# Optimization experiments

Measured on AMD Instinct MI355X. Metric: run time of the kernel, lower is better.

## Reference

```python
import jax, jax.numpy as jnp
import numpy as np

H = 1024
B, LK, LQ = 16, 2048, 64


def setup_inputs() -> dict:
    key0 = jax.random.key(0)
    ks = jax.random.split(key0, 16)
    f = jax.random.normal
    return {
        "query": f(ks[0], (B, 1, H), jnp.float32),
        "key": f(ks[1], (B, LK, 2 * H), jnp.float32),
        "value": f(ks[2], (B, LK, 2 * H), jnp.float32),
        "mask": jax.random.randint(ks[3], (B, 1, LK), 0, 2).astype(jnp.int32),
        "q_key": f(ks[4], (B, LQ, 2 * H), jnp.float32),
        "q_value": f(ks[5], (B, LQ, 2 * H), jnp.float32),
        "q_mask": jax.random.randint(ks[6], (B, 1, LQ), 0, 2).astype(jnp.int32),
        "alphas_state": jax.random.uniform(ks[7], (B, 1, LK), jnp.float32),
        "q_alphas_state": jax.random.uniform(ks[8], (B, 1, LQ), jnp.float32),
        # nn.Linear params: W is [out, in], y = x @ W.T + b
        "W_q": f(ks[9], (2 * H, H + 2 * H + 1), jnp.float32) * 0.02,
        "b_q": jnp.zeros((2 * H,), jnp.float32),
        "W_t": f(ks[10], (2 * H, H + 2 * H + 1 + 2 * H), jnp.float32) * 0.02,
        "b_t": jnp.zeros((2 * H,), jnp.float32),
        "query_other": jax.random.uniform(ks[11], (1, 2 * H), jnp.float32, minval=-0.005, maxval=0.005),
        "text_other": jax.random.uniform(ks[12], (1, 2 * H), jnp.float32, minval=-0.005, maxval=0.005),
    }


def reference(query, key, value, mask, q_key, q_value, q_mask,
              alphas_state, q_alphas_state,
              W_q, b_q, W_t, b_t, query_other, text_other):
    neg_inf = jnp.float32(-jnp.inf)
    Bq, Lq, _ = q_key.shape
    Bk, Lk, _ = key.shape
    # ---- query-side additive attention ----
    qrep = jnp.broadcast_to(query, (Bq, Lq, query.shape[-1]))            # repeat(1, Lq, 1)
    feat = jnp.concatenate([q_key, qrep, q_alphas_state.reshape(Bq, Lq, 1)], axis=-1)
    h = jnp.tanh(jnp.einsum('bli,oi->blo', feat, W_q) + b_q)             # [B, Lq, 2H]
    scores = jnp.einsum('blo,o->bl', h, query_other[0])[:, None, :]      # fused per-batch loop -> [B,1,Lq]
    scores = jnp.where(q_mask == 0, neg_inf, scores)
    q_alphas = jax.nn.softmax(scores, axis=-1)
    query_loss = jnp.sum(jnp.min(
        jnp.concatenate([q_alphas_state[:, 0, :], q_alphas[:, 0, :]], axis=0), axis=0))
    q_context = jnp.einsum('bql,bld->bqd', q_alphas, q_value)            # bmm -> [B,1,2H]
    # ---- text-side additive attention ----
    qrep_k = jnp.broadcast_to(query, (Bk, Lk, query.shape[-1]))
    ctx_rep = jnp.broadcast_to(q_context, (Bk, Lk, q_context.shape[-1]))
    feat_t = jnp.concatenate([key, qrep_k, alphas_state.reshape(Bk, Lk, 1), ctx_rep], axis=-1)
    h_t = jnp.tanh(jnp.einsum('bli,oi->blo', feat_t, W_t) + b_t)         # [B, Lk, 2H]
    scores_t = jnp.einsum('blo,o->bl', h_t, text_other[0])[:, None, :]   # [B,1,Lk]
    scores_t = jnp.where(mask == 0, neg_inf, scores_t)
    alphas = jax.nn.softmax(scores_t, axis=-1)
    text_loss = jnp.sum(jnp.min(
        jnp.concatenate([alphas_state[:, 0, :], alphas[:, 0, :]], axis=0), axis=0))
    context = jnp.einsum('bql,bld->bqd', alphas, value)                  # [B,1,2H]
    return (context, alphas, q_alphas, text_loss, query_loss)
```

## Files before the change

kernel.cpp:

```cpp
#include <hip/hip_runtime.h>
#include <hip/hip_bf16.h>
#include <math.h>

#define GK 2048
#define NCB 16

typedef __attribute__((ext_vector_type(8))) short bf16x8;
typedef __attribute__((ext_vector_type(4))) float f32x4;
typedef __attribute__((ext_vector_type(4))) float f4v;
typedef __attribute__((ext_vector_type(4))) unsigned short u16x4;
typedef __attribute__((ext_vector_type(8))) unsigned short u16x8;

__device__ __forceinline__ unsigned short f2bf(float x) {
    unsigned int u = __float_as_uint(x);
    u += 0x7fffu + ((u >> 16) & 1u);
    return (unsigned short)(u >> 16);
}

__device__ __forceinline__ void gl_lds16(const void* g, void* l) {
    __builtin_amdgcn_global_load_lds(
        (const __attribute__((address_space(1))) unsigned int*)g,
        (__attribute__((address_space(3))) unsigned int*)l, 16, 0, 0);
}

__global__ void prep_kernel(const float* __restrict__ Wt, const float* __restrict__ Wq,
                            const float* __restrict__ q_key, const float* __restrict__ key,
                            const float* __restrict__ query, const float* __restrict__ b_q,
                            unsigned short* __restrict__ Wtk, unsigned short* __restrict__ Wqk,
                            unsigned short* __restrict__ qkb, unsigned short* __restrict__ keyb,
                            float* __restrict__ w3q, float* __restrict__ w3t,
                            float* __restrict__ Dq) {
    int b = blockIdx.x, tid = threadIdx.x;
    if (b < 32768) {
        long i = ((long)b << 11) + (tid << 3);
        f4v a = *(const f4v*)(key + i);
        f4v c = *(const f4v*)(key + i + 4);
        u16x8 r;
        r[0] = f2bf(a[0]); r[1] = f2bf(a[1]); r[2] = f2bf(a[2]); r[3] = f2bf(a[3]);
        r[4] = f2bf(c[0]); r[5] = f2bf(c[1]); r[6] = f2bf(c[2]); r[7] = f2bf(c[3]);
        *(u16x8*)(keyb + i) = r;
        return;
    }
    int b2 = b - 32768;
    if (b2 < 2048) {
        const float* s = Wt + (size_t)b2 * 5121;
        unsigned short* d = Wtk + (size_t)b2 * 2048;
#pragma unroll
        for (int k = 0; k < 8; k++) { int c = tid + (k << 8); d[c] = f2bf(s[c]); }
    } else if (b2 < 4096) {
        int o = b2 - 2048;
        const float* s = Wq + (size_t)o * 3073;
        unsigned short* d = Wqk + (size_t)o * 2048;
#pragma unroll
        for (int k = 0; k < 8; k++) { int c = tid + (k << 8); d[c] = f2bf(s[c]); }
    } else if (b2 < 5120) {
        long i = ((long)(b2 - 4096) * 256 + tid) * 8;
        f4v a = *(const f4v*)(q_key + i);
        f4v c = *(const f4v*)(q_key + i + 4);
        u16x8 r;
        r[0] = f2bf(a[0]); r[1] = f2bf(a[1]); r[2] = f2bf(a[2]); r[3] = f2bf(a[3]);
        r[4] = f2bf(c[0]); r[5] = f2bf(c[1]); r[6] = f2bf(c[2]); r[7] = f2bf(c[3]);
        *(u16x8*)(qkb + i) = r;
    } else if (b2 < 5128) {
        int o = (b2 - 5120) * 256 + tid;
        w3q[o] = Wq[(size_t)o * 3073 + 3072];
        w3t[o] = Wt[(size_t)o * 5121 + 3072];
    } else {
        int wave = tid >> 6, lane = tid & 63;
        int o = (b2 - 5128) * 4 + wave;
        const float* wrow = Wq + (size_t)o * 3073 + 2048;
        float acc[16];
#pragma unroll
        for (int z = 0; z < 16; z++) acc[z] = 0.f;
        for (int i = lane; i < 1024; i += 64) {
            float wv = wrow[i];
            const float* qp = query + i;
#pragma unroll
            for (int z = 0; z < 16; z++) acc[z] += wv * qp[z * 1024];
        }
#pragma unroll
        for (int z = 0; z < 16; z++) {
            float v = acc[z];
            for (int off = 1; off < 64; off <<= 1) v += __shfl_xor(v, off);
            if (lane == 0) Dq[(z << 11) + o] = v + b_q[o];
        }
    }
}

template <int KLEN>
__global__ __launch_bounds__(256) void dconst_kernel(
    const float* __restrict__ W, long ldw,
    const float* __restrict__ bias,
    const float* __restrict__ query,
    const float* __restrict__ qctx,
    float* __restrict__ Dout) {
    int tid = threadIdx.x;
    int wave = tid >> 6, lane = tid & 63;
    int o = blockIdx.x * 4 + wave;
    const float* wrow = W + (size_t)o * ldw + 2048;
    float acc[16];
#pragma unroll
    for (int b2 = 0; b2 < 16; b2++) acc[b2] = 0.f;
    for (int i = lane; i < KLEN; i += 64) {
        if (KLEN == 1024 || i < 1024) {
            float wv = wrow[i];
            const float* qp = query + i;
#pragma unroll
            for (int b2 = 0; b2 < 16; b2++) acc[b2] += wv * qp[b2 * 1024];
        } else {
            float wv = wrow[i + 1];
            const float* cp = qctx + (i - 1024);
#pragma unroll
            for (int b2 = 0; b2 < 16; b2++) acc[b2] += wv * cp[b2 * 2048];
        }
    }
#pragma unroll
    for (int b2 = 0; b2 < 16; b2++) {
        float v = acc[b2];
        for (int off = 1; off < 64; off <<= 1) v += __shfl_xor(v, off);
        if (lane == 0) Dout[(b2 << 11) + o] = v + bias[o];
    }
}

template <int LOG_RPB>
__global__ __launch_bounds__(256) void gemm_score(
    const unsigned short* __restrict__ A,
    const unsigned short* __restrict__ Bt,
    const float* __restrict__ Dc,
    const float* __restrict__ avec,
    const float* __restrict__ w3,
    const float* __restrict__ tvec,
    float* __restrict__ partial,
    int row0) {
    __shared__ unsigned short As[128 * 32];
    __shared__ unsigned short Bs[128 * 32];
    __shared__ float red[128][2];

    int nwg = gridDim.x;
    int bid = blockIdx.x;
    int q8 = nwg >> 3;
    int wg = (bid & 7) * q8 + (bid >> 3);
    int rb = wg >> 4, cb = wg & 15;

    int tid = threadIdx.x;
    int wave = tid >> 6, lane = tid & 63;
    int wr = wave >> 1, wc = wave & 1;
    int l15 = lane & 15, lhi = lane >> 4;

    const unsigned short* Ab = A + (size_t)rb * 128 * GK;
    const unsigned short* Bb = Bt + (size_t)cb * 128 * GK;

    int r0 = tid >> 2, c0 = (tid & 3) << 3;

    f32x4 acc[4][4];
#pragma unroll
    for (int i = 0; i < 4; i++)
#pragma unroll
        for (int j = 0; j < 4; j++) acc[i][j] = (f32x4)0.f;

    unsigned short* AsW0 = As + (wave << 9);
    unsigned short* AsW1 = As + 2048 + (wave << 9);
    unsigned short* BsW0 = Bs + (wave << 9);
    unsigned short* BsW1 = Bs + 2048 + (wave << 9);

    for (int k0 = 0; k0 < GK; k0 += 32) {
        __syncthreads();
        gl_lds16(Ab + (size_t)r0 * GK + k0 + c0, AsW0);
        gl_lds16(Ab + (size_t)(r0 + 64) * GK + k0 + c0, AsW1);
        gl_lds16(Bb + (size_t)r0 * GK + k0 + c0, BsW0);
        gl_lds16(Bb + (size_t)(r0 + 64) * GK + k0 + c0, BsW1);
        __syncthreads();
        bf16x8 a[4], b[4];
#pragma unroll
        for (int mi = 0; mi < 4; mi++)
            a[mi] = *(const bf16x8*)(As + (((wr << 6) + (mi << 4) + l15) << 5) + (lhi << 3));
#pragma unroll
        for (int ni = 0; ni < 4; ni++)
            b[ni] = *(const bf16x8*)(Bs + (((wc << 6) + (ni << 4) + l15) << 5) + (lhi << 3));
#pragma unroll
        for (int mi = 0; mi < 4; mi++)
#pragma unroll
            for (int ni = 0; ni < 4; ni++)
                acc[mi][ni] = __builtin_amdgcn_mfma_f32_16x16x32_bf16(a[mi], b[ni], acc[mi][ni], 0, 0, 0);
    }

    int grow_base = row0 + (rb << 7) + (wr << 6);
    int bb = grow_base >> LOG_RPB;
    int gcol = (cb << 7) + (wc << 6) + l15;
    float Dco[4], w3o[4], tv[4];
#pragma unroll
    for (int ni = 0; ni < 4; ni++) {
        int o = gcol + (ni << 4);
        Dco[ni] = Dc[(bb << 11) + o];
        w3o[ni] = w3[o];
        tv[ni] = tvec[o];
    }
#pragma unroll
    for (int mi = 0; mi < 4; mi++) {
#pragma unroll
        for (int j = 0; j < 4; j++) {
            int rloc = (mi << 4) + (lhi << 2) + j;
            float av = avec[grow_base + rloc];
            float s = 0.f;
#pragma unroll
            for (int ni = 0; ni < 4; ni++) {
                float x = acc[mi][ni][j] + Dco[ni] + av * w3o[ni];
                x = fminf(fmaxf(x, -15.f), 15.f);
                float e = __expf(2.f * x);
                s += ((e - 1.f) / (e + 1.f)) * tv[ni];
            }
#pragma unroll
            for (int off = 1; off < 16; off <<= 1) s += __shfl_xor(s, off);
            if (l15 == 0) red[(wr << 6) + rloc][wc] = s;
        }
    }
    __syncthreads();
    if (tid < 128) {
        partial[(size_t)(row0 + (rb << 7) + tid) * NCB + cb] = red[tid][0] + red[tid][1];
    }
}

#define MFMA16(A, B, C) __builtin_amdgcn_mfma_f32_16x16x32_bf16(A, B, C, 0, 0, 0)

#define STAGE2(GB, GR0, K0, LB) do { \
    int _rr = lane >> 3; \
    int _cc = ((lane & 7) ^ _rr) << 3; \
    gl_lds16((GB) + (size_t)((GR0) + (wid << 3) + _rr) * GK + (K0) + _cc, lds + (LB) + (wid << 9)); \
    gl_lds16((GB) + (size_t)((GR0) + 64 + (wid << 3) + _rr) * GK + (K0) + _cc, lds + (LB) + 4096 + (wid << 9)); \
  } while (0)

#define WAIT4 do { asm volatile("s_waitcnt vmcnt(4)" ::: "memory"); __builtin_amdgcn_sched_barrier(0); } while (0)
#define NOWAIT do { } while (0)

#define PHASE(YOFF, Q, FIRSTB, STAGE_STMT, BOUNDARY) do { \
    bf16x8 a00, a01, a10, a11; \
    if (FIRSTB) { \
        b00 = *(const bf16x8*)(lds8 + bB0[0] + (YOFF)); b01 = *(const bf16x8*)(lds8 + bB1[0] + (YOFF)); \
        b10 = *(const bf16x8*)(lds8 + bB0[1] + (YOFF)); b11 = *(const bf16x8*)(lds8 + bB1[1] + (YOFF)); \
        b20 = *(const bf16x8*)(lds8 + bB0[2] + (YOFF)); b21 = *(const bf16x8*)(lds8 + bB1[2] + (YOFF)); \
        b30 = *(const bf16x8*)(lds8 + bB0[3] + (YOFF)); b31 = *(const bf16x8*)(lds8 + bB1[3] + (YOFF)); \
    } \
    a00 = *(const bf16x8*)(lds8 + aA0[2*(Q)  ] + (YOFF)); a01 = *(const bf16x8*)(lds8 + aA1[2*(Q)  ] + (YOFF)); \
    a10 = *(const bf16x8*)(lds8 + aA0[2*(Q)+1] + (YOFF)); a11 = *(const bf16x8*)(lds8 + aA1[2*(Q)+1] + (YOFF)); \
    STAGE_STMT; \
    BOUNDARY; \
    __builtin_amdgcn_s_barrier(); \
    asm volatile("s_waitcnt lgkmcnt(0)" ::: "memory"); \
    __builtin_amdgcn_sched_barrier(0); \
    __builtin_amdgcn_s_setprio(1); \
    acc[2*(Q)  ][0] = MFMA16(a00, b00, acc[2*(Q)  ][0]); \
    acc[2*(Q)  ][0] = MFMA16(a01, b01, acc[2*(Q)  ][0]); \
    acc[2*(Q)  ][1] = MFMA16(a00, b10, acc[2*(Q)  ][1]); \
    acc[2*(Q)  ][1] = MFMA16(a01, b11, acc[2*(Q)  ][1]); \
    acc[2*(Q)  ][2] = MFMA16(a00, b20, acc[2*(Q)  ][2]); \
    acc[2*(Q)  ][2] = MFMA16(a01, b21, acc[2*(Q)  ][2]); \
    acc[2*(Q)  ][3] = MFMA16(a00, b30, acc[2*(Q)  ][3]); \
    acc[2*(Q)  ][3] = MFMA16(a01, b31, acc[2*(Q)  ][3]); \
    acc[2*(Q)+1][0] = MFMA16(a10, b00, acc[2*(Q)+1][0]); \
    acc[2*(Q)+1][0] = MFMA16(a11, b01, acc[2*(Q)+1][0]); \
    acc[2*(Q)+1][1] = MFMA16(a10, b10, acc[2*(Q)+1][1]); \
    acc[2*(Q)+1][1] = MFMA16(a11, b11, acc[2*(Q)+1][1]); \
    acc[2*(Q)+1][2] = MFMA16(a10, b20, acc[2*(Q)+1][2]); \
    acc[2*(Q)+1][2] = MFMA16(a11, b21, acc[2*(Q)+1][2]); \
    acc[2*(Q)+1][3] = MFMA16(a10, b30, acc[2*(Q)+1][3]); \
    acc[2*(Q)+1][3] = MFMA16(a11, b31, acc[2*(Q)+1][3]); \
    __builtin_amdgcn_s_setprio(0); \
  } while (0)

__global__ __launch_bounds__(512, 2) void gemm256(
    const unsigned short* __restrict__ A,
    const unsigned short* __restrict__ Bt,
    const float* __restrict__ Dc,
    const float* __restrict__ avec,
    const float* __restrict__ w3,
    const float* __restrict__ tvec,
    float* __restrict__ partial) {
    extern __shared__ unsigned short lds[];
    char* lds8 = (char*)lds;
    const int XA = 0, YA = 16384, XB = 32768, YB = 49152;

    int nwg = gridDim.x;
    int bid = blockIdx.x;
    int q8 = nwg >> 3;
    int wg = (bid & 7) * q8 + (bid >> 3);
    int rb = wg >> 3, cb = wg & 7;

    int tid = threadIdx.x;
    int wid = tid >> 6, lane = tid & 63;
    int wr = wid >> 2, wc = wid & 3;
    int l15 = lane & 15, lhi = lane >> 4;

    const unsigned short* Aq = A;
    const unsigned short* Bq = Bt;
    int arow = rb << 8;
    int brow = cb << 8;

    int sw0 = ((lhi ^ (l15 & 7)) << 4);
    int sw1 = (((4 | lhi) ^ (l15 & 7)) << 4);
    int aA0[8], aA1[8], bB0[4], bB1[4];
#pragma unroll
    for (int mi = 0; mi < 8; mi++) {
        int r = (wr << 7) + (mi << 4) + l15;
        aA0[mi] = (r << 7) + sw0;
        aA1[mi] = (r << 7) + sw1;
    }
#pragma unroll
    for (int ni = 0; ni < 4; ni++) {
        int r = (wc << 6) + (ni << 4) + l15;
        bB0[ni] = 65536 + (r << 7) + sw0;
        bB1[ni] = 65536 + (r << 7) + sw1;
    }

    f32x4 acc[8][4];
#pragma unroll
    for (int i = 0; i < 8; i++)
#pragma unroll
        for (int j = 0; j < 4; j++) acc[i][j] = (f32x4)0.f;

    bf16x8 b00, b01, b10, b11, b20, b21, b30, b31;

    STAGE2(Bq, brow, 0, XB);
    STAGE2(Bq, brow + 128, 0, XB + 8192);
    STAGE2(Aq, arow, 0, XA);
    STAGE2(Aq, arow + 128, 0, XA + 8192);
    STAGE2(Bq, brow, 64, YB);
    STAGE2(Bq, brow + 128, 64, YB + 8192);
    asm volatile("s_waitcnt vmcnt(4)" ::: "memory");
    __builtin_amdgcn_sched_barrier(0);
    __builtin_amdgcn_s_barrier();

    for (int it = 0; it < 16; ++it) {
        int k1 = ((it << 1) + 1) << 6;
        int k2 = (((it << 1) + 2) << 6) & 2047;
        int k3 = (((it << 1) + 3) << 6) & 2047;
        PHASE(0,     0, 1, STAGE2(Aq, arow,       k1, YA),        NOWAIT);
        PHASE(0,     1, 0, STAGE2(Aq, arow + 128, k1, YA + 8192), NOWAIT);
        PHASE(0,     2, 0, STAGE2(Bq, brow,       k2, XB),        NOWAIT);
        PHASE(0,     3, 0, STAGE2(Bq, brow + 128, k2, XB + 8192), WAIT4);
        PHASE(32768, 0, 1, STAGE2(Aq, arow,       k2, XA),        NOWAIT);
        PHASE(32768, 1, 0, STAGE2(Aq, arow + 128, k2, XA + 8192), NOWAIT);
        PHASE(32768, 2, 0, STAGE2(Bq, brow,       k3, YB),        NOWAIT);
        PHASE(32768, 3, 0, STAGE2(Bq, brow + 128, k3, YB + 8192), WAIT4);
    }

    int gcolb = (cb << 8) + (wc << 6) + l15;
    int bb = rb >> 3;
    float Dco[4], w3o[4], tv[4];
#pragma unroll
    for (int ni = 0; ni < 4; ++ni) {
        int o = gcolb + (ni << 4);
        Dco[ni] = Dc[(bb << 11) + o];
        w3o[ni] = w3[o];
        tv[ni] = tvec[o];
    }
    float* red = (float*)(lds + 65536);
#pragma unroll
    for (int mi = 0; mi < 8; ++mi) {
#pragma unroll
        for (int j = 0; j < 4; ++j) {
            int rloc = (wr << 7) + (mi << 4) + (lhi << 2) + j;
            float av = avec[(rb << 8) + rloc];
            float s = 0.f;
#pragma unroll
            for (int ni = 0; ni < 4; ++ni) {
                float x = acc[mi][ni][j] + Dco[ni] + av * w3o[ni];
                x = fminf(fmaxf(x, -15.f), 15.f);
                float e = __expf(2.f * x);
                s += ((e - 1.f) / (e + 1.f)) * tv[ni];
            }
#pragma unroll
            for (int off2 = 1; off2 < 16; off2 <<= 1) s += __shfl_xor(s, off2);
            if (l15 == 0) red[(rloc << 2) + wc] = s;
        }
    }
    __syncthreads();
    if (tid < 256) {
        partial[(size_t)((rb << 8) + tid) * 8 + cb] =
            red[(tid << 2)] + red[(tid << 2) + 1] + red[(tid << 2) + 2] + red[(tid << 2) + 3];
    }
}

__global__ void softmax_q_alphas(const float* __restrict__ partial_q,
                                 const int* __restrict__ q_mask,
                                 float* __restrict__ out_qalphas) {
    int b = blockIdx.x, tid = threadIdx.x;
    float s = 0.f;
    const float* p = partial_q + (size_t)(b * 64 + tid) * NCB;
#pragma unroll
    for (int c = 0; c < 16; c++) s += p[c];
    if (q_mask[b * 64 + tid] == 0) s = -INFINITY;
    float m = s;
    for (int off = 1; off < 64; off <<= 1) m = fmaxf(m, __shfl_xor(m, off));
    float e = (s == -INFINITY) ? 0.f : __expf(s - m);
    float sum = e;
    for (int off = 1; off < 64; off <<= 1) sum += __shfl_xor(sum, off);
    out_qalphas[b * 64 + tid] = e / sum;
}

__global__ __launch_bounds__(256) void qctx_kernel(
    const float* __restrict__ qal, const float* __restrict__ q_value,
    float* __restrict__ qctx) {
    int b = blockIdx.x, dc = blockIdx.y, tid = threadIdx.x;
    __shared__ float sal[64];
    if (tid < 64) sal[tid] = qal[b * 64 + tid];
    __syncthreads();
    int d = (dc << 8) + tid;
    float acc = 0.f;
    for (int l = 0; l < 64; l++) {
        float al = sal[l];
        if (al != 0.f) acc += al * q_value[((size_t)(b * 64 + l) << 11) + d];
    }
    qctx[(b << 11) + d] = acc;
}

__global__ __launch_bounds__(256) void softmax_t_kernel(
    const float* __restrict__ partial,
    const int* __restrict__ mask,
    float* __restrict__ out_alphas) {
    int b = blockIdx.x, tid = threadIdx.x;
    int wave = tid >> 6, lane = tid & 63;
    __shared__ float sred[4];
    float sc[8];
    float lm = -INFINITY;
#pragma unroll
    for (int i = 0; i < 8; i++) {
        int l = tid + (i << 8);
        const float* p = partial + (size_t)(b * 2048 + l) * 8;
        float s = 0.f;
#pragma unroll
        for (int c = 0; c < 8; c++) s += p[c];
        if (mask[b * 2048 + l] == 0) s = -INFINITY;
        sc[i] = s;
        lm = fmaxf(lm, s);
    }
    for (int off = 1; off < 64; off <<= 1) lm = fmaxf(lm, __shfl_xor(lm, off));
    if (lane == 0) sred[wave] = lm;
    __syncthreads();
    float m = fmaxf(fmaxf(sred[0], sred[1]), fmaxf(sred[2], sred[3]));
    float ee[8];
    float ls = 0.f;
#pragma unroll
    for (int i = 0; i < 8; i++) {
        ee[i] = (sc[i] == -INFINITY) ? 0.f : __expf(sc[i] - m);
        ls += ee[i];
    }
    for (int off = 1; off < 64; off <<= 1) ls += __shfl_xor(ls, off);
    __syncthreads();
    if (lane == 0) sred[wave] = ls;
    __syncthreads();
    float S = sred[0] + sred[1] + sred[2] + sred[3];
    float inv = 1.f / S;
#pragma unroll
    for (int i = 0; i < 8; i++)
        out_alphas[b * 2048 + tid + (i << 8)] = ee[i] * inv;
}

__global__ __launch_bounds__(256) void ctx_partial_kernel(
    const float* __restrict__ alphas,
    const float* __restrict__ value,
    float* __restrict__ pctx) {
    int b = blockIdx.x, lc = blockIdx.y, tid = threadIdx.x;
    __shared__ float sa[64];
    if (tid < 64) sa[tid] = alphas[(b << 11) + (lc << 6) + tid];
    __syncthreads();
    f4v a0 = (f4v)0.f, a1 = (f4v)0.f;
    const float* vb = value + ((size_t)((b << 11) + (lc << 6)) << 11);
    for (int l = 0; l < 64; l++) {
        float al = sa[l];
        if (al != 0.f) {
            const f4v* vr = (const f4v*)(vb + ((size_t)l << 11));
            a0 += al * vr[tid];
            a1 += al * vr[tid + 256];
        }
    }
    f4v* p = (f4v*)(pctx + ((size_t)((b << 5) + lc) << 11));
    p[tid] = a0;
    p[tid + 256] = a1;
}

__global__ __launch_bounds__(256) void ctx_reduce_kernel(
    const float* __restrict__ pctx, float* __restrict__ out_ctx) {
    int b = blockIdx.x, half = blockIdx.y, tid = threadIdx.x;
    int d4 = (half << 8) + tid;
    f4v s = (f4v)0.f;
#pragma unroll
    for (int lc = 0; lc < 32; lc++)
        s += ((const f4v*)(pctx + ((size_t)((b << 5) + lc) << 11)))[d4];
    ((f4v*)(out_ctx + ((size_t)b << 11)))[d4] = s;
}

__global__ void loss_part_kernel(const float* __restrict__ qs, const float* __restrict__ qa,
                                 const float* __restrict__ ts, const float* __restrict__ ta,
                                 float* __restrict__ parts) {
    int blk = blockIdx.x, tid = threadIdx.x;
    int wave = tid >> 6, lane = tid & 63;
    __shared__ float sred[2];
    float s = 0.f;
    if (blk == 0) {
        if (tid < 64) {
            float m = INFINITY;
#pragma unroll
            for (int b = 0; b < 16; ++b) {
                m = fminf(m, qs[(b << 6) + tid]);
                m = fminf(m, qa[(b << 6) + tid]);
            }
            s = m;
        }
    } else {
        int l = ((blk - 1) << 7) + tid;
        float m = INFINITY;
#pragma unroll
        for (int b = 0; b < 16; ++b) {
            m = fminf(m, ts[(b << 11) + l]);
            m = fminf(m, ta[(b << 11) + l]);
        }
        s = m;
    }
    for (int off = 1; off < 64; off <<= 1) s += __shfl_xor(s, off);
    if (lane == 0) sred[wave] = s;
    __syncthreads();
    if (tid == 0) parts[blk] = sred[0] + sred[1];
}

__global__ void loss_final_kernel(const float* __restrict__ parts,
                                  float* __restrict__ out_tl, float* __restrict__ out_ql) {
    if (threadIdx.x == 0) {
        *out_ql = parts[0];
        float t = 0.f;
        for (int i = 1; i <= 16; ++i) t += parts[i];
        *out_tl = t;
    }
}

extern "C" void kernel_launch(void* const* d_in, const int* in_sizes, int n_in,
                              void* d_out, int out_size, void* d_ws, size_t ws_size,
                              hipStream_t stream) {
    const float* query          = (const float*)d_in[0];
    const float* key            = (const float*)d_in[1];
    const float* value          = (const float*)d_in[2];
    const int*   mask           = (const int*)d_in[3];
    const float* q_key          = (const float*)d_in[4];
    const float* q_value        = (const float*)d_in[5];
    const int*   q_mask         = (const int*)d_in[6];
    const float* alphas_state   = (const float*)d_in[7];
    const float* q_alphas_state = (const float*)d_in[8];
    const float* W_q            = (const float*)d_in[9];
    const float* b_q            = (const float*)d_in[10];
    const float* W_t            = (const float*)d_in[11];
    const float* b_t            = (const float*)d_in[12];
    const float* query_other    = (const float*)d_in[13];
    const float* text_other     = (const float*)d_in[14];

    float* out        = (float*)d_out;
    float* out_ctx     = out;
    float* out_alphas  = out + 32768;
    float* out_qalphas = out + 65536;
    float* out_tloss   = out + 66560;
    float* out_qloss   = out + 66561;

    char* w = (char*)d_ws;
    size_t off = 0;
    auto alloc = [&](size_t bytes) -> char* {
        char* p = w + off;
        off += (bytes + 255) & ~(size_t)255;
        return p;
    };
    unsigned short* Wtk  = (unsigned short*)alloc(2048ull * 2048 * 2);
    unsigned short* Wqk  = (unsigned short*)alloc(2048ull * 2048 * 2);
    unsigned short* qkb  = (unsigned short*)alloc(1024ull * 2048 * 2);
    unsigned short* keyb = (unsigned short*)alloc(32768ull * 2048 * 2);
    float* partial_t     = (float*)alloc(32768ull * 8 * 4);
    float* partial_q     = (float*)alloc(1024ull * NCB * 4);
    float* Dq            = (float*)alloc(16 * 2048 * 4);
    float* Dt            = (float*)alloc(16 * 2048 * 4);
    float* qctx          = (float*)alloc(16 * 2048 * 4);
    float* w3q           = (float*)alloc(2048 * 4);
    float* w3t           = (float*)alloc(2048 * 4);
    float* pctx          = (float*)alloc(16ull * 32 * 2048 * 4);
    float* lparts        = (float*)alloc(32 * 4);

    hipFuncSetAttribute((const void*)gemm256,
                        hipFuncAttributeMaxDynamicSharedMemorySize, 135168);

    prep_kernel<<<38408, 256, 0, stream>>>(W_t, W_q, q_key, key, query, b_q,
                                           Wtk, Wqk, qkb, keyb, w3q, w3t, Dq);

    gemm_score<6><<<128, 256, 0, stream>>>(qkb, Wqk, Dq, q_alphas_state, w3q,
                                           query_other, partial_q, 0);
    softmax_q_alphas<<<16, 64, 0, stream>>>(partial_q, q_mask, out_qalphas);
    qctx_kernel<<<dim3(16, 8), 256, 0, stream>>>(out_qalphas, q_value, qctx);

    dconst_kernel<3072><<<512, 256, 0, stream>>>(W_t, 5121, b_t, query, qctx, Dt);
    gemm256<<<1024, 512, 135168, stream>>>(keyb, Wtk, Dt, alphas_state, w3t,
                                           text_other, partial_t);

    softmax_t_kernel<<<16, 256, 0, stream>>>(partial_t, mask, out_alphas);
    ctx_partial_kernel<<<dim3(16, 32), 256, 0, stream>>>(out_alphas, value, pctx);
    ctx_reduce_kernel<<<dim3(16, 2), 256, 0, stream>>>(pctx, out_ctx);
    loss_part_kernel<<<17, 128, 0, stream>>>(q_alphas_state, out_qalphas,
                                             alphas_state, out_alphas, lparts);
    loss_final_kernel<<<1, 64, 0, stream>>>(lparts, out_tloss, out_qloss);
}
```

Baseline: 483.8 us.

## Fuse fp32-to-bf16 key conversion into main GEMM with triple-buffered fp32 A tiles

Removes the separate pass that converted the large key tensor (32768x2048 fp32) to bf16. The main GEMM now streams fp32 key tiles straight into LDS and converts them in registers with packed bf16 conversion instructions before the MFMAs. The K loop is restructured to 32-wide K steps with a three-stage LDS ring buffer. This eliminates a full read-convert-write round trip of the key tensor, at the cost of double-size A tiles in LDS, more LDS space (151552 bytes), and extra conversion ALU work inside the inner loop.

```diff
diff --git a/kernel.cpp b/kernel.cpp
--- a/kernel.cpp
+++ b/kernel.cpp
@@ -10,6 +10,7 @@
 typedef __attribute__((ext_vector_type(4))) float f4v;
 typedef __attribute__((ext_vector_type(4))) unsigned short u16x4;
 typedef __attribute__((ext_vector_type(8))) unsigned short u16x8;
+typedef __attribute__((ext_vector_type(4))) unsigned int u32x4;
 
 __device__ __forceinline__ unsigned short f2bf(float x) {
     unsigned int u = __float_as_uint(x);
@@ -23,25 +24,24 @@
         (__attribute__((address_space(3))) unsigned int*)l, 16, 0, 0);
 }
 
+__device__ __forceinline__ bf16x8 cvt8(f32x4 lo, f32x4 hi) {
+    unsigned int w0, w1, w2, w3;
+    asm("v_cvt_pk_bf16_f32 %0, %1, %2" : "=v"(w0) : "v"(lo[0]), "v"(lo[1]));
+    asm("v_cvt_pk_bf16_f32 %0, %1, %2" : "=v"(w1) : "v"(lo[2]), "v"(lo[3]));
+    asm("v_cvt_pk_bf16_f32 %0, %1, %2" : "=v"(w2) : "v"(hi[0]), "v"(hi[1]));
+    asm("v_cvt_pk_bf16_f32 %0, %1, %2" : "=v"(w3) : "v"(hi[2]), "v"(hi[3]));
+    u32x4 t; t[0] = w0; t[1] = w1; t[2] = w2; t[3] = w3;
+    return *(bf16x8*)&t;
+}
+
 __global__ void prep_kernel(const float* __restrict__ Wt, const float* __restrict__ Wq,
-                            const float* __restrict__ q_key, const float* __restrict__ key,
+                            const float* __restrict__ q_key,
                             const float* __restrict__ query, const float* __restrict__ b_q,
                             unsigned short* __restrict__ Wtk, unsigned short* __restrict__ Wqk,
-                            unsigned short* __restrict__ qkb, unsigned short* __restrict__ keyb,
+                            unsigned short* __restrict__ qkb,
                             float* __restrict__ w3q, float* __restrict__ w3t,
                             float* __restrict__ Dq) {
-    int b = blockIdx.x, tid = threadIdx.x;
-    if (b < 32768) {
-        long i = ((long)b << 11) + (tid << 3);
-        f4v a = *(const f4v*)(key + i);
-        f4v c = *(const f4v*)(key + i + 4);
-        u16x8 r;
-        r[0] = f2bf(a[0]); r[1] = f2bf(a[1]); r[2] = f2bf(a[2]); r[3] = f2bf(a[3]);
-        r[4] = f2bf(c[0]); r[5] = f2bf(c[1]); r[6] = f2bf(c[2]); r[7] = f2bf(c[3]);
-        *(u16x8*)(keyb + i) = r;
-        return;
-    }
-    int b2 = b - 32768;
+    int b2 = blockIdx.x, tid = threadIdx.x;
     if (b2 < 2048) {
         const float* s = Wt + (size_t)b2 * 5121;
         unsigned short* d = Wtk + (size_t)b2 * 2048;
@@ -222,53 +222,71 @@
 
 #define MFMA16(A, B, C) __builtin_amdgcn_mfma_f32_16x16x32_bf16(A, B, C, 0, 0, 0)
 
-#define STAGE2(GB, GR0, K0, LB) do { \
-    int _rr = lane >> 3; \
-    int _cc = ((lane & 7) ^ _rr) << 3; \
-    gl_lds16((GB) + (size_t)((GR0) + (wid << 3) + _rr) * GK + (K0) + _cc, lds + (LB) + (wid << 9)); \
-    gl_lds16((GB) + (size_t)((GR0) + 64 + (wid << 3) + _rr) * GK + (K0) + _cc, lds + (LB) + 4096 + (wid << 9)); \
+#define STG_A(K0, LBb) do { \
+    int _r0 = (wid << 5) + (lane >> 3); \
+    int _gc = ((lane & 7) ^ (lane >> 3)) << 2; \
+    gl_lds16(A32 + (size_t)(arow + _r0)      * GK + (K0) + _gc, lds8 + (LBb) + (wid << 12)        + (lane << 4)); \
+    gl_lds16(A32 + (size_t)(arow + _r0 + 8)  * GK + (K0) + _gc, lds8 + (LBb) + (wid << 12) + 1024 + (lane << 4)); \
+    gl_lds16(A32 + (size_t)(arow + _r0 + 16) * GK + (K0) + _gc, lds8 + (LBb) + (wid << 12) + 2048 + (lane << 4)); \
+    gl_lds16(A32 + (size_t)(arow + _r0 + 24) * GK + (K0) + _gc, lds8 + (LBb) + (wid << 12) + 3072 + (lane << 4)); \
   } while (0)
 
-#define WAIT4 do { asm volatile("s_waitcnt vmcnt(4)" ::: "memory"); __builtin_amdgcn_sched_barrier(0); } while (0)
-#define NOWAIT do { } while (0)
-
-#define PHASE(YOFF, Q, FIRSTB, STAGE_STMT, BOUNDARY) do { \
-    bf16x8 a00, a01, a10, a11; \
-    if (FIRSTB) { \
-        b00 = *(const bf16x8*)(lds8 + bB0[0] + (YOFF)); b01 = *(const bf16x8*)(lds8 + bB1[0] + (YOFF)); \
-        b10 = *(const bf16x8*)(lds8 + bB0[1] + (YOFF)); b11 = *(const bf16x8*)(lds8 + bB1[1] + (YOFF)); \
-        b20 = *(const bf16x8*)(lds8 + bB0[2] + (YOFF)); b21 = *(const bf16x8*)(lds8 + bB1[2] + (YOFF)); \
-        b30 = *(const bf16x8*)(lds8 + bB0[3] + (YOFF)); b31 = *(const bf16x8*)(lds8 + bB1[3] + (YOFF)); \
+#define STG_B(K0, LBb) do { \
+    int _r0 = (wid << 5) + (lane >> 2); \
+    int _gc = ((lane & 3) ^ ((lane >> 2) & 3)) << 3; \
+    gl_lds16(Bt + (size_t)(brow + _r0)      * GK + (K0) + _gc, lds8 + (LBb) + (wid << 11)        + (lane << 4)); \
+    gl_lds16(Bt + (size_t)(brow + _r0 + 16) * GK + (K0) + _gc, lds8 + (LBb) + (wid << 11) + 1024 + (lane << 4)); \
+  } while (0)
+
+#define VM6 do { asm volatile("s_waitcnt vmcnt(6)" ::: "memory"); __builtin_amdgcn_sched_barrier(0); } while (0)
+
+#define PH(Ab, Bb, Q, ...) do { \
+    f32x4 g0 = *(const f32x4*)(lds8 + (Ab) + rA[4*(Q)  ] + colo); \
+    f32x4 h0 = *(const f32x4*)(lds8 + (Ab) + rA[4*(Q)  ] + cohi); \
+    f32x4 g1 = *(const f32x4*)(lds8 + (Ab) + rA[4*(Q)+1] + colo); \
+    f32x4 h1 = *(const f32x4*)(lds8 + (Ab) + rA[4*(Q)+1] + cohi); \
+    f32x4 g2 = *(const f32x4*)(lds8 + (Ab) + rA[4*(Q)+2] + colo); \
+    f32x4 h2 = *(const f32x4*)(lds8 + (Ab) + rA[4*(Q)+2] + cohi); \
+    f32x4 g3 = *(const f32x4*)(lds8 + (Ab) + rA[4*(Q)+3] + colo); \
+    f32x4 h3 = *(const f32x4*)(lds8 + (Ab) + rA[4*(Q)+3] + cohi); \
+    if ((Q) == 0) { \
+        b0 = *(const bf16x8*)(lds8 + (Bb) + rB[0]); \
+        b1 = *(const bf16x8*)(lds8 + (Bb) + rB[1]); \
+        b2 = *(const bf16x8*)(lds8 + (Bb) + rB[2]); \
+        b3 = *(const bf16x8*)(lds8 + (Bb) + rB[3]); \
     } \
-    a00 = *(const bf16x8*)(lds8 + aA0[2*(Q)  ] + (YOFF)); a01 = *(const bf16x8*)(lds8 + aA1[2*(Q)  ] + (YOFF)); \
-    a10 = *(const bf16x8*)(lds8 + aA0[2*(Q)+1] + (YOFF)); a11 = *(const bf16x8*)(lds8 + aA1[2*(Q)+1] + (YOFF)); \
-    STAGE_STMT; \
-    BOUNDARY; \
-    __builtin_amdgcn_s_barrier(); \
+    __VA_ARGS__; \
     asm volatile("s_waitcnt lgkmcnt(0)" ::: "memory"); \
     __builtin_amdgcn_sched_barrier(0); \
+    bf16x8 a0 = cvt8(g0, h0); \
+    bf16x8 a1 = cvt8(g1, h1); \
+    bf16x8 a2 = cvt8(g2, h2); \
+    bf16x8 a3 = cvt8(g3, h3); \
+    __builtin_amdgcn_s_barrier(); \
     __builtin_amdgcn_s_setprio(1); \
-    acc[2*(Q)  ][0] = MFMA16(a00, b00, acc[2*(Q)  ][0]); \
-    acc[2*(Q)  ][0] = MFMA16(a01, b01, acc[2*(Q)  ][0]); \
-    acc[2*(Q)  ][1] = MFMA16(a00, b10, acc[2*(Q)  ][1]); \
-    acc[2*(Q)  ][1] = MFMA16(a01, b11, acc[2*(Q)  ][1]); \
-    acc[2*(Q)  ][2] = MFMA16(a00, b20, acc[2*(Q)  ][2]); \
-    acc[2*(Q)  ][2] = MFMA16(a01, b21, acc[2*(Q)  ][2]); \
-    acc[2*(Q)  ][3] = MFMA16(a00, b30, acc[2*(Q)  ][3]); \
-    acc[2*(Q)  ][3] = MFMA16(a01, b31, acc[2*(Q)  ][3]); \
-    acc[2*(Q)+1][0] = MFMA16(a10, b00, acc[2*(Q)+1][0]); \
-    acc[2*(Q)+1][0] = MFMA16(a11, b01, acc[2*(Q)+1][0]); \
-    acc[2*(Q)+1][1] = MFMA16(a10, b10, acc[2*(Q)+1][1]); \
-    acc[2*(Q)+1][1] = MFMA16(a11, b11, acc[2*(Q)+1][1]); \
-    acc[2*(Q)+1][2] = MFMA16(a10, b20, acc[2*(Q)+1][2]); \
-    acc[2*(Q)+1][2] = MFMA16(a11, b21, acc[2*(Q)+1][2]); \
-    acc[2*(Q)+1][3] = MFMA16(a10, b30, acc[2*(Q)+1][3]); \
-    acc[2*(Q)+1][3] = MFMA16(a11, b31, acc[2*(Q)+1][3]); \
+    acc[4*(Q)  ][0] = MFMA16(a0, b0, acc[4*(Q)  ][0]); \
+    acc[4*(Q)  ][1] = MFMA16(a0, b1, acc[4*(Q)  ][1]); \
+    acc[4*(Q)  ][2] = MFMA16(a0, b2, acc[4*(Q)  ][2]); \
+    acc[4*(Q)  ][3] = MFMA16(a0, b3, acc[4*(Q)  ][3]); \
+    acc[4*(Q)+1][0] = MFMA16(a1, b0, acc[4*(Q)+1][0]); \
+    acc[4*(Q)+1][1] = MFMA16(a1, b1, acc[4*(Q)+1][1]); \
+    acc[4*(Q)+1][2] = MFMA16(a1, b2, acc[4*(Q)+1][2]); \
+    acc[4*(Q)+1][3] = MFMA16(a1, b3, acc[4*(Q)+1][3]); \
+    acc[4*(Q)+2][0] = MFMA16(a2, b0, acc[4*(Q)+2][0]); \
+    acc[4*(Q)+2][1] = MFMA16(a2, b1, acc[4*(Q)+2][1]); \
+    acc[4*(Q)+2][2] = MFMA16(a2, b2, acc[4*(Q)+2][2]); \
+    acc[4*(Q)+2][3] = MFMA16(a2, b3, acc[4*(Q)+2][3]); \
+    acc[4*(Q)+3][0] = MFMA16(a3, b0, acc[4*(Q)+3][0]); \
+    acc[4*(Q)+3][1] = MFMA16(a3, b1, acc[4*(Q)+3][1]); \
+    acc[4*(Q)+3][2] = MFMA16(a3, b2, acc[4*(Q)+3][2]); \
+    acc[4*(Q)+3][3] = MFMA16(a3, b3, acc[4*(Q)+3][3]); \
     __builtin_amdgcn_s_setprio(0); \
   } while (0)
 
+#define TILE(Ab, Bb, SA, SB) do { PH(Ab, Bb, 0, SA); PH(Ab, Bb, 1, SB); } while (0)
+
 __global__ __launch_bounds__(512, 2) void gemm256(
-    const unsigned short* __restrict__ A,
+    const float* __restrict__ A32,
     const unsigned short* __restrict__ Bt,
     const float* __restrict__ Dc,
     const float* __restrict__ avec,
@@ -277,7 +295,8 @@
     float* __restrict__ partial) {
     extern __shared__ unsigned short lds[];
     char* lds8 = (char*)lds;
-    const int XA = 0, YA = 16384, XB = 32768, YB = 49152;
+    const int A0b = 0, A1b = 32768, A2b = 65536;
+    const int B0b = 98304, B1b = 114688, B2b = 131072;
 
     int nwg = gridDim.x;
     int bid = blockIdx.x;
@@ -290,26 +309,18 @@
     int wr = wid >> 2, wc = wid & 3;
     int l15 = lane & 15, lhi = lane >> 4;
 
-    const unsigned short* Aq = A;
-    const unsigned short* Bq = Bt;
     int arow = rb << 8;
     int brow = cb << 8;
 
-    int sw0 = ((lhi ^ (l15 & 7)) << 4);
-    int sw1 = (((4 | lhi) ^ (l15 & 7)) << 4);
-    int aA0[8], aA1[8], bB0[4], bB1[4];
-#pragma unroll
-    for (int mi = 0; mi < 8; mi++) {
-        int r = (wr << 7) + (mi << 4) + l15;
-        aA0[mi] = (r << 7) + sw0;
-        aA1[mi] = (r << 7) + sw1;
-    }
-#pragma unroll
-    for (int ni = 0; ni < 4; ni++) {
-        int r = (wc << 6) + (ni << 4) + l15;
-        bB0[ni] = 65536 + (r << 7) + sw0;
-        bB1[ni] = 65536 + (r << 7) + sw1;
-    }
+    int rA[8], rB[4];
+#pragma unroll
+    for (int mi = 0; mi < 8; mi++)
+        rA[mi] = ((wr << 7) + (mi << 4) + l15) << 7;
+    int colo = (((lhi << 1) ^ (l15 & 7)) << 4);
+    int cohi = ((((lhi << 1) | 1) ^ (l15 & 7)) << 4);
+#pragma unroll
+    for (int ni = 0; ni < 4; ni++)
+        rB[ni] = (((wc << 6) + (ni << 4) + l15) << 6) + ((lhi ^ (l15 & 3)) << 4);
 
     f32x4 acc[8][4];
 #pragma unroll
@@ -317,31 +328,23 @@
 #pragma unroll
         for (int j = 0; j < 4; j++) acc[i][j] = (f32x4)0.f;
 
-    bf16x8 b00, b01, b10, b11, b20, b21, b30, b31;
-
-    STAGE2(Bq, brow, 0, XB);
-    STAGE2(Bq, brow + 128, 0, XB + 8192);
-    STAGE2(Aq, arow, 0, XA);
-    STAGE2(Aq, arow + 128, 0, XA + 8192);
-    STAGE2(Bq, brow, 64, YB);
-    STAGE2(Bq, brow + 128, 64, YB + 8192);
-    asm volatile("s_waitcnt vmcnt(4)" ::: "memory");
+    bf16x8 b0, b1, b2, b3;
+
+    STG_A(0, A0b);  STG_B(0, B0b);
+    STG_A(32, A1b); STG_B(32, B1b);
+    asm volatile("s_waitcnt vmcnt(6)" ::: "memory");
     __builtin_amdgcn_sched_barrier(0);
     __builtin_amdgcn_s_barrier();
 
-    for (int it = 0; it < 16; ++it) {
-        int k1 = ((it << 1) + 1) << 6;
-        int k2 = (((it << 1) + 2) << 6) & 2047;
-        int k3 = (((it << 1) + 3) << 6) & 2047;
-        PHASE(0,     0, 1, STAGE2(Aq, arow,       k1, YA),        NOWAIT);
-        PHASE(0,     1, 0, STAGE2(Aq, arow + 128, k1, YA + 8192), NOWAIT);
-        PHASE(0,     2, 0, STAGE2(Bq, brow,       k2, XB),        NOWAIT);
-        PHASE(0,     3, 0, STAGE2(Bq, brow + 128, k2, XB + 8192), WAIT4);
-        PHASE(32768, 0, 1, STAGE2(Aq, arow,       k2, XA),        NOWAIT);
-        PHASE(32768, 1, 0, STAGE2(Aq, arow + 128, k2, XA + 8192), NOWAIT);
-        PHASE(32768, 2, 0, STAGE2(Bq, brow,       k3, YB),        NOWAIT);
-        PHASE(32768, 3, 0, STAGE2(Bq, brow + 128, k3, YB + 8192), WAIT4);
-    }
+    for (int it = 0; it < 21; ++it) {
+        int ka = (it * 96 + 64) & 2047;
+        int kb = (it * 96 + 96) & 2047;
+        int kc = (it * 96 + 128) & 2047;
+        TILE(A0b, B0b, STG_A(ka, A2b), { STG_B(ka, B2b); VM6; });
+        TILE(A1b, B1b, STG_A(kb, A0b), { STG_B(kb, B0b); VM6; });
+        TILE(A2b, B2b, STG_A(kc, A1b), { STG_B(kc, B1b); VM6; });
+    }
+    TILE(A0b, B0b, (void)0, (void)0);
 
     int gcolb = (cb << 8) + (wc << 6) + l15;
     int bb = rb >> 3;
@@ -353,7 +356,7 @@
         w3o[ni] = w3[o];
         tv[ni] = tvec[o];
     }
-    float* red = (float*)(lds + 65536);
+    float* red = (float*)(lds8 + 147456);
 #pragma unroll
     for (int mi = 0; mi < 8; ++mi) {
 #pragma unroll
@@ -568,7 +571,6 @@
     unsigned short* Wtk  = (unsigned short*)alloc(2048ull * 2048 * 2);
     unsigned short* Wqk  = (unsigned short*)alloc(2048ull * 2048 * 2);
     unsigned short* qkb  = (unsigned short*)alloc(1024ull * 2048 * 2);
-    unsigned short* keyb = (unsigned short*)alloc(32768ull * 2048 * 2);
     float* partial_t     = (float*)alloc(32768ull * 8 * 4);
     float* partial_q     = (float*)alloc(1024ull * NCB * 4);
     float* Dq            = (float*)alloc(16 * 2048 * 4);
@@ -580,10 +582,10 @@
     float* lparts        = (float*)alloc(32 * 4);
 
     hipFuncSetAttribute((const void*)gemm256,
-                        hipFuncAttributeMaxDynamicSharedMemorySize, 135168);
-
-    prep_kernel<<<38408, 256, 0, stream>>>(W_t, W_q, q_key, key, query, b_q,
-                                           Wtk, Wqk, qkb, keyb, w3q, w3t, Dq);
+                        hipFuncAttributeMaxDynamicSharedMemorySize, 151552);
+
+    prep_kernel<<<5640, 256, 0, stream>>>(W_t, W_q, q_key, query, b_q,
+                                          Wtk, Wqk, qkb, w3q, w3t, Dq);
 
     gemm_score<6><<<128, 256, 0, stream>>>(qkb, Wqk, Dq, q_alphas_state, w3q,
                                            query_other, partial_q, 0);
@@ -591,7 +593,7 @@
     qctx_kernel<<<dim3(16, 8), 256, 0, stream>>>(out_qalphas, q_value, qctx);
 
     dconst_kernel<3072><<<512, 256, 0, stream>>>(W_t, 5121, b_t, query, qctx, Dt);
-    gemm256<<<1024, 512, 135168, stream>>>(keyb, Wtk, Dt, alphas_state, w3t,
+    gemm256<<<1024, 512, 151552, stream>>>(key, Wtk, Dt, alphas_state, w3t,
                                            text_other, partial_t);
 
     softmax_t_kernel<<<16, 256, 0, stream>>>(partial_t, mask, out_alphas);
```

New measurement: 510.4 us. +5.5%, slower.
